# Performance work log

Measured on AMD Instinct MI355X. Metric: run time of the kernel, lower is better.

Reference implementation:

```python
import jax, jax.numpy as jnp
import numpy as np

N_NODES = 50000
N_EDGES = 800000
D_FEAT = 64
IN_DIM = 1 + 2 * D_FEAT  # 129
FC_DIMS = [128, 64, 1]


def setup_inputs() -> dict:
    key = jax.random.key(0)
    ks = jax.random.split(key, 10)
    x = jax.random.normal(ks[0], (N_NODES, D_FEAT), dtype=jnp.float32)
    edge_index = jax.random.randint(ks[1], (2, N_EDGES), 0, N_NODES, dtype=jnp.int64)
    edge_weight = jax.random.uniform(ks[2], (N_EDGES, 1), dtype=jnp.float32)
    # MLP params (Linear: y = x @ W.T + b), Kaiming-ish scale
    dims = [IN_DIM] + FC_DIMS
    W1 = jax.random.normal(ks[3], (dims[1], dims[0]), dtype=jnp.float32) / np.sqrt(dims[0])
    b1 = jnp.zeros((dims[1],), dtype=jnp.float32)
    W2 = jax.random.normal(ks[4], (dims[2], dims[1]), dtype=jnp.float32) / np.sqrt(dims[1])
    b2 = jnp.zeros((dims[2],), dtype=jnp.float32)
    W3 = jax.random.normal(ks[5], (dims[3], dims[2]), dtype=jnp.float32) / np.sqrt(dims[2])
    b3 = jnp.zeros((dims[3],), dtype=jnp.float32)
    return {"x": x, "edge_index": edge_index, "edge_weight": edge_weight,
            "W1": W1, "b1": b1, "W2": W2, "b2": b2, "W3": W3, "b3": b3}


def reference(x, edge_index, edge_weight, W1, b1, W2, b2, W3, b3):
    # Gather source/target node features per edge: [E, d]
    src = x[edge_index[0]]
    tgt = x[edge_index[1]]
    # Concat [edge_weight | src | tgt] -> [E, 1 + 2d]
    h = jnp.concatenate([edge_weight, src, tgt], axis=1)
    # MLP (dropout is None / eval; last layer dim==1 -> no ReLU)
    h = jax.nn.relu(h @ W1.T + b1)
    h = jax.nn.relu(h @ W2.T + b2)
    return h @ W3.T + b3  # [E, 1] new edge weights
```

## Files before the change

### kernel.cpp

```cpp
#include <hip/hip_runtime.h>

typedef _Float16 half8 __attribute__((ext_vector_type(8)));
typedef _Float16 half4_t __attribute__((ext_vector_type(4)));
typedef float floatx4 __attribute__((ext_vector_type(4)));

#define LP 136

__global__ __launch_bounds__(256) void repack_weights(
    const float* __restrict__ W1, const float* __restrict__ W2,
    _Float16* __restrict__ wsh)
{
    int tid = blockIdx.x * 256 + threadIdx.x;
    if (tid < 16384) {
        int c = tid >> 9, r = tid & 511;
        int L = r >> 3, jj = r & 7;
        int mt = c >> 2, kb = c & 3;
        int n = mt * 16 + (L & 15);
        int k = kb * 32 + (L >> 4) * 8 + jj;
        wsh[tid] = (_Float16)W1[n * 129 + 1 + k];
    } else if (tid < 24576) {
        int t = tid - 16384;
        int c = t >> 9, r = t & 511;
        int L = r >> 3, jj = r & 7;
        int mt = c >> 2, kb = c & 3;
        int i = mt * 16 + (L & 15);
        int j = kb * 32 + (L >> 4) * 8 + jj;
        wsh[tid] = (_Float16)W2[i * 128 + j];
    }
}

__global__ __launch_bounds__(256, 2) void edge_mlp_kernel(
    const float* __restrict__ x,
    const int* __restrict__ ei,
    const float* __restrict__ ew,
    const float* __restrict__ W1, const float* __restrict__ b1,
    const float* __restrict__ b2,
    const float* __restrict__ W3, const float* __restrict__ b3,
    const _Float16* __restrict__ wf,
    float* __restrict__ out, int E)
{
    __shared__ __align__(16) _Float16 hA[64 * LP];
    __shared__ __align__(16) _Float16 h1A[64 * LP];
    __shared__ float s_ew[64];
    __shared__ float s_b1[128];
    __shared__ float s_c0[128];
    __shared__ float s_b2[64];
    __shared__ float s_w3[64];
    __shared__ float s_out[4][64];

    const int tid = threadIdx.x;
    const int e_blk = blockIdx.x * 64;

    if (tid < 128) { s_b1[tid] = b1[tid]; s_c0[tid] = W1[tid * 129]; }
    else if (tid < 192) { int i = tid - 128; s_b2[i] = b2[i]; s_w3[i] = W3[i]; }
    if (tid < 64) {
        int e = e_blk + tid; if (e >= E) e = E - 1;
        s_ew[tid] = ew[e];
    }

    {
        int e_loc = tid >> 2;
        int part = tid & 3;
        int e = e_blk + e_loc; if (e >= E) e = E - 1;
        int nsrc = ei[e];
        int ntgt = ei[E + e];
        const float* rowp = (part < 2) ? (x + (long long)nsrc * 64)
                                       : (x + (long long)ntgt * 64);
        const float* pp = rowp + (part & 1) * 32;
        _Float16* dst = &hA[e_loc * LP + part * 32];
#pragma unroll
        for (int q = 0; q < 8; ++q) {
            float4 v = *(const float4*)(pp + q * 4);
            half4_t h = { (_Float16)v.x, (_Float16)v.y, (_Float16)v.z, (_Float16)v.w };
            *(half4_t*)(dst + q * 4) = h;
        }
    }
    __syncthreads();

    const int lane = tid & 63;
    const int wave = tid >> 6;
    const int lrow = lane & 15;
    const int quad = lane >> 4;

    half8 bfr[4][4];
#pragma unroll
    for (int nt = 0; nt < 4; ++nt)
#pragma unroll
        for (int kb = 0; kb < 4; ++kb)
            bfr[nt][kb] = *(const half8*)(&hA[(nt * 16 + lrow) * LP + kb * 32 + quad * 8]);

    floatx4 acc1[2][4];
#pragma unroll
    for (int mi = 0; mi < 2; ++mi) {
        half8 afr[4];
#pragma unroll
        for (int kb = 0; kb < 4; ++kb)
            afr[kb] = *(const half8*)(wf + ((2 * wave + mi) * 4 + kb) * 512 + lane * 8);
#pragma unroll
        for (int nt = 0; nt < 4; ++nt) {
            floatx4 a = {0.f, 0.f, 0.f, 0.f};
#pragma unroll
            for (int kb = 0; kb < 4; ++kb)
                a = __builtin_amdgcn_mfma_f32_16x16x32_f16(afr[kb], bfr[nt][kb], a, 0, 0, 0);
            acc1[mi][nt] = a;
        }
    }

#pragma unroll
    for (int mi = 0; mi < 2; ++mi) {
        int nb = (2 * wave + mi) * 16 + quad * 4;
#pragma unroll
        for (int nt = 0; nt < 4; ++nt) {
            int e = nt * 16 + lrow;
            float ewv = s_ew[e];
            half4_t hv;
#pragma unroll
            for (int r = 0; r < 4; ++r) {
                float v = acc1[mi][nt][r] + s_b1[nb + r] + ewv * s_c0[nb + r];
                v = fmaxf(v, 0.f);
                hv[r] = (_Float16)v;
            }
            *(half4_t*)(&h1A[e * LP + nb]) = hv;
        }
    }
    __syncthreads();

    half8 b2fr[4][4];
#pragma unroll
    for (int nt = 0; nt < 4; ++nt)
#pragma unroll
        for (int kb = 0; kb < 4; ++kb)
            b2fr[nt][kb] = *(const half8*)(&h1A[(nt * 16 + lrow) * LP + kb * 32 + quad * 8]);

    half8 a2fr[4];
#pragma unroll
    for (int kb = 0; kb < 4; ++kb)
        a2fr[kb] = *(const half8*)(wf + 16384 + (wave * 4 + kb) * 512 + lane * 8);

#pragma unroll
    for (int nt = 0; nt < 4; ++nt) {
        floatx4 a = {0.f, 0.f, 0.f, 0.f};
#pragma unroll
        for (int kb = 0; kb < 4; ++kb)
            a = __builtin_amdgcn_mfma_f32_16x16x32_f16(a2fr[kb], b2fr[nt][kb], a, 0, 0, 0);
        int ib = wave * 16 + quad * 4;
        float p = 0.f;
#pragma unroll
        for (int r = 0; r < 4; ++r) {
            float v = a[r] + s_b2[ib + r];
            v = fmaxf(v, 0.f);
            p += v * s_w3[ib + r];
        }
        p += __shfl_xor(p, 16, 64);
        p += __shfl_xor(p, 32, 64);
        if (quad == 0) s_out[wave][nt * 16 + lrow] = p;
    }
    __syncthreads();

    if (tid < 64) {
        int oe = e_blk + tid;
        if (oe < E)
            out[oe] = b3[0] + s_out[0][tid] + s_out[1][tid]
                            + s_out[2][tid] + s_out[3][tid];
    }
}

extern "C" void kernel_launch(void* const* d_in, const int* in_sizes, int n_in,
                              void* d_out, int out_size, void* d_ws, size_t ws_size,
                              hipStream_t stream) {
    const float* x  = (const float*)d_in[0];
    const int*   ei = (const int*)d_in[1];
    const float* ew = (const float*)d_in[2];
    const float* W1 = (const float*)d_in[3];
    const float* b1 = (const float*)d_in[4];
    const float* W2 = (const float*)d_in[5];
    const float* b2 = (const float*)d_in[6];
    const float* W3 = (const float*)d_in[7];
    const float* b3 = (const float*)d_in[8];
    float* out = (float*)d_out;
    const int E = in_sizes[2];
    _Float16* wsh = (_Float16*)d_ws;

    repack_weights<<<96, 256, 0, stream>>>(W1, W2, wsh);
    int nblk = (E + 63) / 64;
    edge_mlp_kernel<<<nblk, 256, 0, stream>>>(x, ei, ew, W1, b1, b2, W3, b3,
                                              wsh, out, E);
}
```

Baseline: 171.5 us.

## Pre-convert node features to fp16 and process 128 edges per block

A prep kernel now converts the whole x table to fp16 in workspace, alongside the weight repack. The edge kernel then gathers half-precision rows, halving gather bytes per edge. Each block handles 128 edges and reuses one LDS buffer for both layers, with tighter launch bounds to raise occupancy. This adds a full pass over x each call and more register pressure from holding layer-1 outputs before the LDS write-back.

```diff
diff --git a/kernel.cpp b/kernel.cpp
--- a/kernel.cpp
+++ b/kernel.cpp
@@ -6,31 +6,44 @@
 
 #define LP 136
 
-__global__ __launch_bounds__(256) void repack_weights(
+__global__ __launch_bounds__(256) void prep_kernel(
+    const float* __restrict__ x,
     const float* __restrict__ W1, const float* __restrict__ W2,
-    _Float16* __restrict__ wsh)
+    _Float16* __restrict__ wsh, _Float16* __restrict__ xh, int n_x8)
 {
-    int tid = blockIdx.x * 256 + threadIdx.x;
-    if (tid < 16384) {
-        int c = tid >> 9, r = tid & 511;
-        int L = r >> 3, jj = r & 7;
-        int mt = c >> 2, kb = c & 3;
-        int n = mt * 16 + (L & 15);
-        int k = kb * 32 + (L >> 4) * 8 + jj;
-        wsh[tid] = (_Float16)W1[n * 129 + 1 + k];
-    } else if (tid < 24576) {
-        int t = tid - 16384;
-        int c = t >> 9, r = t & 511;
-        int L = r >> 3, jj = r & 7;
-        int mt = c >> 2, kb = c & 3;
-        int i = mt * 16 + (L & 15);
-        int j = kb * 32 + (L >> 4) * 8 + jj;
-        wsh[tid] = (_Float16)W2[i * 128 + j];
+    int b = blockIdx.x;
+    if (b < 96) {
+        int tid = b * 256 + threadIdx.x;
+        if (tid < 16384) {
+            int c = tid >> 9, r = tid & 511;
+            int L = r >> 3, jj = r & 7;
+            int mt = c >> 2, kb = c & 3;
+            int n = mt * 16 + (L & 15);
+            int k = kb * 32 + (L >> 4) * 8 + jj;
+            wsh[tid] = (_Float16)W1[n * 129 + 1 + k];
+        } else {
+            int t = tid - 16384;
+            int c = t >> 9, r = t & 511;
+            int L = r >> 3, jj = r & 7;
+            int mt = c >> 2, kb = c & 3;
+            int i = mt * 16 + (L & 15);
+            int j = kb * 32 + (L >> 4) * 8 + jj;
+            wsh[tid] = (_Float16)W2[i * 128 + j];
+        }
+    } else {
+        int t2 = (b - 96) * 256 + threadIdx.x;
+        if (t2 < n_x8) {
+            const float4* p = (const float4*)(x + (size_t)t2 * 8);
+            float4 v0 = p[0], v1 = p[1];
+            half8 h = {(_Float16)v0.x, (_Float16)v0.y, (_Float16)v0.z, (_Float16)v0.w,
+                       (_Float16)v1.x, (_Float16)v1.y, (_Float16)v1.z, (_Float16)v1.w};
+            *(half8*)(xh + (size_t)t2 * 8) = h;
+        }
     }
 }
 
-__global__ __launch_bounds__(256, 2) void edge_mlp_kernel(
-    const float* __restrict__ x,
+__global__ __launch_bounds__(256, 4) void edge_mlp_kernel(
+    const _Float16* __restrict__ xh,
     const int* __restrict__ ei,
     const float* __restrict__ ew,
     const float* __restrict__ W1, const float* __restrict__ b1,
@@ -39,41 +52,38 @@
     const _Float16* __restrict__ wf,
     float* __restrict__ out, int E)
 {
-    __shared__ __align__(16) _Float16 hA[64 * LP];
-    __shared__ __align__(16) _Float16 h1A[64 * LP];
-    __shared__ float s_ew[64];
+    __shared__ __align__(16) _Float16 hA[128 * LP];
+    __shared__ float s_ew[128];
     __shared__ float s_b1[128];
     __shared__ float s_c0[128];
     __shared__ float s_b2[64];
     __shared__ float s_w3[64];
-    __shared__ float s_out[4][64];
+    __shared__ float s_out[4][128];
 
     const int tid = threadIdx.x;
-    const int e_blk = blockIdx.x * 64;
+    const int e_blk = blockIdx.x * 128;
 
-    if (tid < 128) { s_b1[tid] = b1[tid]; s_c0[tid] = W1[tid * 129]; }
-    else if (tid < 192) { int i = tid - 128; s_b2[i] = b2[i]; s_w3[i] = W3[i]; }
-    if (tid < 64) {
+    if (tid < 128) {
+        s_b1[tid] = b1[tid];
+        s_c0[tid] = W1[tid * 129];
         int e = e_blk + tid; if (e >= E) e = E - 1;
         s_ew[tid] = ew[e];
+    } else if (tid < 192) {
+        int i = tid - 128;
+        s_b2[i] = b2[i];
+        s_w3[i] = W3[i];
     }
 
     {
-        int e_loc = tid >> 2;
-        int part = tid & 3;
+        int e_loc = tid >> 1;
+        int part = tid & 1;
         int e = e_blk + e_loc; if (e >= E) e = E - 1;
-        int nsrc = ei[e];
-        int ntgt = ei[E + e];
-        const float* rowp = (part < 2) ? (x + (long long)nsrc * 64)
-                                       : (x + (long long)ntgt * 64);
-        const float* pp = rowp + (part & 1) * 32;
-        _Float16* dst = &hA[e_loc * LP + part * 32];
+        int node = ei[(size_t)part * E + e];
+        const _Float16* rp = xh + (size_t)node * 64;
+        _Float16* dst = &hA[e_loc * LP + part * 64];
 #pragma unroll
-        for (int q = 0; q < 8; ++q) {
-            float4 v = *(const float4*)(pp + q * 4);
-            half4_t h = { (_Float16)v.x, (_Float16)v.y, (_Float16)v.z, (_Float16)v.w };
-            *(half4_t*)(dst + q * 4) = h;
-        }
+        for (int q = 0; q < 8; ++q)
+            *(half8*)(dst + q * 8) = *(const half8*)(rp + q * 8);
     }
     __syncthreads();
 
@@ -82,55 +92,47 @@
     const int lrow = lane & 15;
     const int quad = lane >> 4;
 
-    half8 bfr[4][4];
+    half8 afr[2][4];
 #pragma unroll
-    for (int nt = 0; nt < 4; ++nt)
+    for (int mi = 0; mi < 2; ++mi)
 #pragma unroll
         for (int kb = 0; kb < 4; ++kb)
-            bfr[nt][kb] = *(const half8*)(&hA[(nt * 16 + lrow) * LP + kb * 32 + quad * 8]);
+            afr[mi][kb] = *(const half8*)(wf + ((2 * wave + mi) * 4 + kb) * 512 + lane * 8);
 
-    floatx4 acc1[2][4];
+    half4_t h1v[2][8];
 #pragma unroll
-    for (int mi = 0; mi < 2; ++mi) {
-        half8 afr[4];
+    for (int nt = 0; nt < 8; ++nt) {
+        half8 bfr[4];
 #pragma unroll
         for (int kb = 0; kb < 4; ++kb)
-            afr[kb] = *(const half8*)(wf + ((2 * wave + mi) * 4 + kb) * 512 + lane * 8);
+            bfr[kb] = *(const half8*)(&hA[(nt * 16 + lrow) * LP + kb * 32 + quad * 8]);
+        float ewv = s_ew[nt * 16 + lrow];
 #pragma unroll
-        for (int nt = 0; nt < 4; ++nt) {
+        for (int mi = 0; mi < 2; ++mi) {
             floatx4 a = {0.f, 0.f, 0.f, 0.f};
 #pragma unroll
             for (int kb = 0; kb < 4; ++kb)
-                a = __builtin_amdgcn_mfma_f32_16x16x32_f16(afr[kb], bfr[nt][kb], a, 0, 0, 0);
-            acc1[mi][nt] = a;
+                a = __builtin_amdgcn_mfma_f32_16x16x32_f16(afr[mi][kb], bfr[kb], a, 0, 0, 0);
+            int nb = (2 * wave + mi) * 16 + quad * 4;
+            half4_t hv;
+#pragma unroll
+            for (int r = 0; r < 4; ++r) {
+                float v = a[r] + s_b1[nb + r] + ewv * s_c0[nb + r];
+                hv[r] = (_Float16)fmaxf(v, 0.f);
+            }
+            h1v[mi][nt] = hv;
         }
     }
+    __syncthreads();
 
 #pragma unroll
     for (int mi = 0; mi < 2; ++mi) {
         int nb = (2 * wave + mi) * 16 + quad * 4;
 #pragma unroll
-        for (int nt = 0; nt < 4; ++nt) {
-            int e = nt * 16 + lrow;
-            float ewv = s_ew[e];
-            half4_t hv;
-#pragma unroll
-            for (int r = 0; r < 4; ++r) {
-                float v = acc1[mi][nt][r] + s_b1[nb + r] + ewv * s_c0[nb + r];
-                v = fmaxf(v, 0.f);
-                hv[r] = (_Float16)v;
-            }
-            *(half4_t*)(&h1A[e * LP + nb]) = hv;
-        }
+        for (int nt = 0; nt < 8; ++nt)
+            *(half4_t*)(&hA[(nt * 16 + lrow) * LP + nb]) = h1v[mi][nt];
     }
     __syncthreads();
-
-    half8 b2fr[4][4];
-#pragma unroll
-    for (int nt = 0; nt < 4; ++nt)
-#pragma unroll
-        for (int kb = 0; kb < 4; ++kb)
-            b2fr[nt][kb] = *(const half8*)(&h1A[(nt * 16 + lrow) * LP + kb * 32 + quad * 8]);
 
     half8 a2fr[4];
 #pragma unroll
@@ -138,26 +140,27 @@
         a2fr[kb] = *(const half8*)(wf + 16384 + (wave * 4 + kb) * 512 + lane * 8);
 
 #pragma unroll
-    for (int nt = 0; nt < 4; ++nt) {
+    for (int nt = 0; nt < 8; ++nt) {
+        half8 bfr[4];
+#pragma unroll
+        for (int kb = 0; kb < 4; ++kb)
+            bfr[kb] = *(const half8*)(&hA[(nt * 16 + lrow) * LP + kb * 32 + quad * 8]);
         floatx4 a = {0.f, 0.f, 0.f, 0.f};
 #pragma unroll
         for (int kb = 0; kb < 4; ++kb)
-            a = __builtin_amdgcn_mfma_f32_16x16x32_f16(a2fr[kb], b2fr[nt][kb], a, 0, 0, 0);
+            a = __builtin_amdgcn_mfma_f32_16x16x32_f16(a2fr[kb], bfr[kb], a, 0, 0, 0);
         int ib = wave * 16 + quad * 4;
         float p = 0.f;
 #pragma unroll
-        for (int r = 0; r < 4; ++r) {
-            float v = a[r] + s_b2[ib + r];
-            v = fmaxf(v, 0.f);
-            p += v * s_w3[ib + r];
-        }
+        for (int r = 0; r < 4; ++r)
+            p += fmaxf(a[r] + s_b2[ib + r], 0.f) * s_w3[ib + r];
         p += __shfl_xor(p, 16, 64);
         p += __shfl_xor(p, 32, 64);
         if (quad == 0) s_out[wave][nt * 16 + lrow] = p;
     }
     __syncthreads();
 
-    if (tid < 64) {
+    if (tid < 128) {
         int oe = e_blk + tid;
         if (oe < E)
             out[oe] = b3[0] + s_out[0][tid] + s_out[1][tid]
@@ -179,10 +182,16 @@
     const float* b3 = (const float*)d_in[8];
     float* out = (float*)d_out;
     const int E = in_sizes[2];
+    const int n_x = in_sizes[0];
+    const int n_x8 = n_x / 8;
+
     _Float16* wsh = (_Float16*)d_ws;
+    _Float16* xh  = (_Float16*)((char*)d_ws + 49152);
 
-    repack_weights<<<96, 256, 0, stream>>>(W1, W2, wsh);
-    int nblk = (E + 63) / 64;
-    edge_mlp_kernel<<<nblk, 256, 0, stream>>>(x, ei, ew, W1, b1, b2, W3, b3,
+    int xblk = (n_x8 + 255) / 256;
+    prep_kernel<<<96 + xblk, 256, 0, stream>>>(x, W1, W2, wsh, xh, n_x8);
+
+    int nblk = (E + 127) / 128;
+    edge_mlp_kernel<<<nblk, 256, 0, stream>>>(xh, ei, ew, W1, b1, b2, W3, b3,
                                               wsh, out, E);
 }
```

Result: faster. 141.4 us (-17.5%).
